# Kernel tuning notes

Measured on AMD Instinct MI355X. Metric: run time of the kernel, lower is better.

## Reference

```python
import jax, jax.numpy as jnp
import numpy as np

DIM = 128
DIM_OUT = 128
TK = 3   # time kernel (causal)
SK = 3   # spatial kernel
EPS = 1e-8


def setup_inputs() -> dict:
    key = jax.random.key(0)
    k1, k2, k3 = jax.random.split(key, 3)
    fmap = jax.random.normal(k1, (4, DIM, 16, 64, 64), dtype=jnp.float32)
    cond = jax.random.normal(k2, (4, DIM), dtype=jnp.float32)
    fan_in = DIM * TK * SK * SK
    gain = 0.75  # kaiming gain for selu
    weights = jax.random.normal(k3, (DIM_OUT, DIM, TK, SK, SK), dtype=jnp.float32) * (gain / np.sqrt(fan_in))
    return {"fmap": fmap, "cond": cond, "weights": weights}


def reference(fmap, cond, weights):
    # per-sample weight modulation: w[b,o,i,kt,kh,kw] = W[o,i,...] * (cond[b,i] + 1)
    w = weights[None] * (cond[:, None, :, None, None, None] + 1.0)
    # demodulation: normalize per (b, o) over (i, kt, kh, kw)
    ssq = jnp.sum(w * w, axis=(2, 3, 4, 5), keepdims=True)
    w = w * jax.lax.rsqrt(jnp.maximum(ssq, EPS))
    # causal time padding (TK-1, 0), symmetric spatial padding SK//2
    sp = SK // 2
    fmap_p = jnp.pad(fmap, ((0, 0), (0, 0), (TK - 1, 0), (sp, sp), (sp, sp)))
    # per-sample conv3d (equivalent to groups=b grouped conv)
    dn = ('NCDHW', 'OIDHW', 'NCDHW')
    def conv_one(x, wi):
        # x: [c, t, h, w], wi: [o, i, kt, kh, kw]
        return jax.lax.conv_general_dilated(
            x[None], wi, window_strides=(1, 1, 1), padding='VALID',
            dimension_numbers=dn)[0]
    return jax.vmap(conv_one)(fmap_p, w)  # [b, o, t, h, w]
```

## Files before the change

kernel.cpp:

```cpp
#include <hip/hip_runtime.h>

typedef float f32x4 __attribute__((ext_vector_type(4)));
typedef short s16x8 __attribute__((ext_vector_type(8)));

#define NB 4
#define CIN 128
#define COUT 128
#define NT 16
#define NH 64
#define NW 64
#define NTAP 27
#define KTOT (CIN * NTAP)

#define FT_H 66
#define FT_W 66
#define WMOD_BYTES (NB * NTAP * COUT * CIN * 2)
#define FT_U16 ((size_t)NB * NT * FT_H * FT_W * CIN)
#define FT_BYTES (FT_U16 * 2)
#define WS_NEED ((size_t)WMOD_BYTES + FT_BYTES)

#define SFT 4
#define SFH 6
#define SFW 72
#define SFPX (SFT * SFH * SFW)
#define SF_SLOTS (SFPX * 4)
#define SW_U16 (COUT * 32)

__device__ __forceinline__ unsigned short f32_to_bf16(float f) {
    unsigned int u = __builtin_bit_cast(unsigned int, f);
    u += 0x7FFFu + ((u >> 16) & 1u);
    return (unsigned short)(u >> 16);
}

__device__ __forceinline__ void gload16(const void* g, void* l) {
    __builtin_amdgcn_global_load_lds(
        (const __attribute__((address_space(1))) unsigned int*)g,
        (__attribute__((address_space(3))) unsigned int*)l, 16, 0, 0);
}

__global__ __launch_bounds__(256) void modw_kernel(
    const float* __restrict__ cond,
    const float* __restrict__ weights,
    unsigned short* __restrict__ wmod,
    int swz)
{
    int bo = blockIdx.x;
    int b = bo >> 7;
    int o = bo & 127;
    int tid = threadIdx.x;
    __shared__ float red[256];
    __shared__ float s_scale;
    const float* wrow = weights + o * KTOT;
    const float* cb = cond + b * CIN;

    float acc = 0.f;
    for (int idx = tid; idx < KTOT; idx += 256) {
        int i = idx / NTAP;
        float v = wrow[idx] * (cb[i] + 1.0f);
        acc += v * v;
    }
    red[tid] = acc;
    __syncthreads();
    #pragma unroll
    for (int s = 128; s > 0; s >>= 1) {
        if (tid < s) red[tid] += red[tid + s];
        __syncthreads();
    }
    if (tid == 0) s_scale = 1.0f / sqrtf(fmaxf(red[0], 1e-8f));
    __syncthreads();
    float scale = s_scale;
    int sw_o = swz ? ((o >> 1) & 3) : 0;

    for (int idx = tid; idx < KTOT; idx += 256) {
        int i = idx / NTAP;
        int tap = idx - i * NTAP;
        float v = wrow[idx] * (cb[i] + 1.0f) * scale;
        int pos = (i & 0x60) | ((((i >> 3) & 3) ^ sw_o) << 3) | (i & 7);
        wmod[(((b * NTAP + tap) * COUT + o) * CIN) + pos] = f32_to_bf16(v);
    }
}

__global__ void border_kernel(unsigned short* __restrict__ fmapT) {
    int idx = blockIdx.x * blockDim.x + threadIdx.x;
    int total = NB * NT * 260 * 16;
    if (idx >= total) return;
    int slot = idx & 15;
    int pid = idx >> 4;
    int r = pid % 260;
    int bt = pid / 260;
    int hh, ww;
    if (r < 66)       { hh = 0;  ww = r; }
    else if (r < 132) { hh = 65; ww = r - 66; }
    else if (r < 196) { ww = 0;  hh = r - 131; }
    else              { ww = 65; hh = r - 195; }
    size_t p = (((size_t)bt * FT_H + hh) * FT_W + ww) * CIN + slot * 8;
    uint4 z = {0, 0, 0, 0};
    *reinterpret_cast<uint4*>(&fmapT[p]) = z;
}

__global__ __launch_bounds__(256) void transpose_kernel(
    const float* __restrict__ fmap, unsigned short* __restrict__ fmapT)
{
    __shared__ __attribute__((aligned(16))) unsigned short sT[NW * 136];
    int bid = blockIdx.x;
    int h = bid & 63;
    int t = (bid >> 6) & 15;
    int b = bid >> 10;
    int tid = threadIdx.x;

    int c = tid >> 1, wh = (tid & 1) * 32;
    const float* src = fmap + (((size_t)(b * CIN + c) * NT + t) * NH + h) * NW + wh;
    #pragma unroll
    for (int j = 0; j < 8; ++j) {
        float4 v = *reinterpret_cast<const float4*>(src + j * 4);
        int w = wh + j * 4;
        sT[(w + 0) * 136 + c] = f32_to_bf16(v.x);
        sT[(w + 1) * 136 + c] = f32_to_bf16(v.y);
        sT[(w + 2) * 136 + c] = f32_to_bf16(v.z);
        sT[(w + 3) * 136 + c] = f32_to_bf16(v.w);
    }
    __syncthreads();

    int w = tid >> 2, qq = tid & 3;
    int sw = ((w + 1) >> 1) & 3;
    size_t pixbase = (((size_t)(b * NT + t) * FT_H + (h + 1)) * FT_W + (w + 1)) * CIN;
    #pragma unroll
    for (int s = 0; s < 4; ++s) {
        int g = qq * 4 + s;
        uint4 v = *reinterpret_cast<const uint4*>(&sT[w * 136 + g * 8]);
        int slot = (g & 12) | ((g & 3) ^ sw);
        *reinterpret_cast<uint4*>(&fmapT[pixbase + slot * 8]) = v;
    }
}

__global__ __launch_bounds__(512, 2) void conv2_kernel(
    const unsigned short* __restrict__ fmapT,
    const unsigned short* __restrict__ wmod,
    float* __restrict__ out)
{
    __shared__ __attribute__((aligned(16))) unsigned short sF[SFPX * 32];
    __shared__ __attribute__((aligned(16))) unsigned short sW[2][SW_U16];

    int obid = blockIdx.x;
    int bid = (obid & 7) * 64 + (obid >> 3);
    int h0 = (bid & 15) * 4;
    int t0 = ((bid >> 4) & 7) * 2;
    int b  = bid >> 7;

    int tid = threadIdx.x;
    int wv = tid >> 6;
    int l  = tid & 63;
    int lo = l & 15, hi = l >> 4;
    int obase = (wv & 1) * 64;
    int tsub  = (wv >> 1) & 1;
    int hp    = (wv >> 2) * 2;

    int swzA = (lo >> 1) & 3;

    f32x4 acc[4][2][4];
    f32x4 zz = {0.f, 0.f, 0.f, 0.f};
    #pragma unroll
    for (int a = 0; a < 4; ++a)
        #pragma unroll
        for (int h2 = 0; h2 < 2; ++h2)
            #pragma unroll
            for (int p = 0; p < 4; ++p)
                acc[a][h2][p] = zz;

    int nz = (t0 == 0) ? (2 * SFH * SFW * 4) : 0;

    auto stage_f = [&](int ic) {
        #pragma unroll 1
        for (int j = 0; j < 14; ++j) {
            int s = j * 512 + tid;
            if (s < SF_SLOTS) {
                int px = s >> 2, q = s & 3;
                int row = px / SFW;
                int wl = px - row * SFW;
                int tl = row / SFH;
                int hl = row - tl * SFH;
                int ts = t0 + tl - 2; if (ts < 0) ts = 0;
                int wlc = wl > 65 ? 65 : wl;
                const unsigned short* src = fmapT +
                    ((((size_t)(b * NT + ts) * FT_H + (h0 + hl)) * FT_W + wlc) << 7)
                    + (ic << 5) + (q << 3);
                gload16(src, &sF[(size_t)s * 8]);
            }
        }
    };
    auto stage_w = [&](int buf, int tap, int ic) {
        const unsigned short* src = wmod +
            (((size_t)(b * NTAP + tap) * COUT + (tid >> 2)) << 7)
            + (ic << 5) + ((tid & 3) << 3);
        gload16(src, &sW[buf][tid * 8]);
    };
    auto zero_t = [&]() {
        uint4 z = {0, 0, 0, 0};
        for (int s = tid; s < nz; s += 512)
            *reinterpret_cast<uint4*>(&sF[s * 8]) = z;
    };

    stage_f(0);
    stage_w(0, 0, 0);
    asm volatile("s_waitcnt vmcnt(0)" ::: "memory");
    if (nz) zero_t();
    __syncthreads();

    int tap = 0, kt = 0, kh = 0, kw = 0, ic = 0;
    for (int ks = 0; ks < 108; ++ks) {
        int cur = ks & 1;
        bool last_tap = (tap == NTAP - 1);
        if (!last_tap)
            stage_w(cur ^ 1, tap + 1, ic);

        int swzB = ((lo + kw) >> 1) & 3;
        const unsigned short* wb = &sW[cur][((obase + lo) << 5) + ((hi ^ swzA) << 3)];
        s16x8 af[4];
        #pragma unroll
        for (int a = 0; a < 4; ++a)
            af[a] = *reinterpret_cast<const s16x8*>(&wb[a << 9]);

        #pragma unroll
        for (int h2 = 0; h2 < 2; ++h2) {
            int row = (tsub + kt) * SFH + hp + h2 + kh;
            int pix = row * SFW + kw + lo;
            const unsigned short* fb = &sF[(pix << 5) + ((hi ^ swzB) << 3)];
            s16x8 bf[4];
            #pragma unroll
            for (int p = 0; p < 4; ++p)
                bf[p] = *reinterpret_cast<const s16x8*>(&fb[p << 9]);
            #pragma unroll
            for (int a = 0; a < 4; ++a)
                #pragma unroll
                for (int p = 0; p < 4; ++p)
                    acc[a][h2][p] = __builtin_amdgcn_mfma_f32_16x16x32_bf16(
                        af[a], bf[p], acc[a][h2][p], 0, 0, 0);
        }

        if (!last_tap) {
            ++tap; ++kw;
            if (kw == 3) { kw = 0; ++kh; if (kh == 3) { kh = 0; ++kt; } }
            asm volatile("s_waitcnt vmcnt(0)" ::: "memory");
            __syncthreads();
        } else {
            __syncthreads();
            if (ks < 107) {
                ++ic;
                stage_f(ic);
                stage_w(cur ^ 1, 0, ic);
                asm volatile("s_waitcnt vmcnt(0)" ::: "memory");
                if (nz) zero_t();
                __syncthreads();
            }
            tap = 0; kw = 0; kh = 0; kt = 0;
        }
    }

    int t = t0 + tsub;
    #pragma unroll
    for (int a = 0; a < 4; ++a) {
        #pragma unroll
        for (int h2 = 0; h2 < 2; ++h2) {
            int h = h0 + hp + h2;
            #pragma unroll
            for (int reg = 0; reg < 4; ++reg) {
                int o = obase + a * 16 + hi * 4 + reg;
                float* orow = out + ((((size_t)b * COUT + o) * NT + t) * NH + h) * NW;
                #pragma unroll
                for (int p = 0; p < 4; ++p)
                    orow[p * 16 + lo] = acc[a][h2][p][reg];
            }
        }
    }
}

#define HB 4
#define SF_T 3
#define SF_Hf (HB + 2)
#define SF_Wf (NW + 2)
#define IPAD 40
#define SPATf (SF_T * SF_Hf * SF_Wf)

__global__ __launch_bounds__(512) void conv_kernel(
    const float* __restrict__ fmap,
    const unsigned short* __restrict__ wmod,
    float* __restrict__ out)
{
    __shared__ unsigned short sFf[SPATf * IPAD];
    __shared__ unsigned short sWf[2][COUT * IPAD];

    int bid = blockIdx.x;
    int h0 = (bid & 15) * HB;
    int t0 = (bid >> 4) & 15;
    int b  = bid >> 8;

    int tid = threadIdx.x;
    int wv = tid >> 6;
    int l  = tid & 63;
    int lo = l & 15;
    int hi = l >> 4;
    int obase = (wv & 1) * 64;
    int r = wv >> 1;

    int s_ii = tid >> 4;
    int s_ws = tid & 15;

    f32x4 acc[4][4];
    #pragma unroll
    for (int a = 0; a < 4; ++a)
        #pragma unroll
        for (int p = 0; p < 4; ++p)
            acc[a][p] = f32x4{0.f, 0.f, 0.f, 0.f};

    int tap = 0, icc = 0;
    for (int ks = 0; ks < 108; ++ks) {
        if (tap == 0) {
            if (ks) __syncthreads();
            const float* fbase = fmap + (size_t)((b * CIN + icc * 32 + s_ii) * NT) * (NH * NW);
            for (int e = s_ws; e < SPATf; e += 16) {
                int wl = e % SF_Wf;
                int rr = e / SF_Wf;
                int hl = rr % SF_Hf;
                int tl = rr / SF_Hf;
                int ts = t0 + tl - 2;
                int hs = h0 + hl - 1;
                int wsrc = wl - 1;
                float v = 0.f;
                if (ts >= 0 && (unsigned)hs < NH && (unsigned)wsrc < NW)
                    v = fbase[(ts * NH + hs) * NW + wsrc];
                sFf[e * IPAD + s_ii] = f32_to_bf16(v);
            }
            if (ks == 0) {
                int o = tid >> 2, q = tid & 3;
                const unsigned short* src =
                    wmod + (((b * NTAP + 0) * COUT + o) * CIN) + q * 8;
                *reinterpret_cast<uint4*>(&sWf[0][o * IPAD + q * 8]) =
                    *reinterpret_cast<const uint4*>(src);
            }
        }
        __syncthreads();

        if (ks + 1 < 108) {
            int ksn = ks + 1;
            int icn = ksn / 27;
            int tapn = ksn - icn * 27;
            int o = tid >> 2, q = tid & 3;
            const unsigned short* src =
                wmod + (((b * NTAP + tapn) * COUT + o) * CIN) + icn * 32 + q * 8;
            *reinterpret_cast<uint4*>(&sWf[ksn & 1][o * IPAD + q * 8]) =
                *reinterpret_cast<const uint4*>(src);
        }

        int kt = tap / 9;
        int rem = tap - kt * 9;
        int kh = rem / 3;
        int kw = rem - kh * 3;

        s16x8 af[4], bfr[4];
        #pragma unroll
        for (int a = 0; a < 4; ++a) {
            int o = obase + a * 16 + lo;
            af[a] = *reinterpret_cast<const s16x8*>(&sWf[ks & 1][o * IPAD + hi * 8]);
        }
        #pragma unroll
        for (int p = 0; p < 4; ++p) {
            int sp = (kt * SF_Hf + (r + kh)) * SF_Wf + (p * 16 + lo + kw);
            bfr[p] = *reinterpret_cast<const s16x8*>(&sFf[sp * IPAD + hi * 8]);
        }
        #pragma unroll
        for (int a = 0; a < 4; ++a)
            #pragma unroll
            for (int p = 0; p < 4; ++p)
                acc[a][p] = __builtin_amdgcn_mfma_f32_16x16x32_bf16(
                    af[a], bfr[p], acc[a][p], 0, 0, 0);

        if (++tap == 27) { tap = 0; ++icc; }
    }

    int h = h0 + r;
    #pragma unroll
    for (int a = 0; a < 4; ++a) {
        #pragma unroll
        for (int reg = 0; reg < 4; ++reg) {
            int o = obase + a * 16 + hi * 4 + reg;
            float* orow = out + ((((size_t)b * COUT + o) * NT + t0) * NH + h) * NW;
            #pragma unroll
            for (int p = 0; p < 4; ++p)
                orow[p * 16 + lo] = acc[a][p][reg];
        }
    }
}

extern "C" void kernel_launch(void* const* d_in, const int* in_sizes, int n_in,
                              void* d_out, int out_size, void* d_ws, size_t ws_size,
                              hipStream_t stream) {
    (void)in_sizes; (void)n_in; (void)out_size;
    const float* fmap    = (const float*)d_in[0];
    const float* cond    = (const float*)d_in[1];
    const float* weights = (const float*)d_in[2];
    float* outp = (float*)d_out;
    unsigned short* wmod = (unsigned short*)d_ws;

    if (ws_size >= WS_NEED) {
        unsigned short* fmapT = (unsigned short*)((char*)d_ws + WMOD_BYTES);
        modw_kernel<<<dim3(NB * COUT), dim3(256), 0, stream>>>(cond, weights, wmod, 1);
        border_kernel<<<dim3((NB * NT * 260 * 16 + 255) / 256), dim3(256), 0, stream>>>(fmapT);
        transpose_kernel<<<dim3(NB * NT * NH), dim3(256), 0, stream>>>(fmap, fmapT);
        conv2_kernel<<<dim3(NB * (NT / 2) * (NH / 4)), dim3(512), 0, stream>>>(fmapT, wmod, outp);
    } else {
        modw_kernel<<<dim3(NB * COUT), dim3(256), 0, stream>>>(cond, weights, wmod, 0);
        conv_kernel<<<dim3(NB * NT * (NH / HB)), dim3(512), 0, stream>>>(fmap, wmod, outp);
    }
}
```

Measured before the change: 298.6 us.

## Triple-buffer weight tiles with vmcnt(1) prefetch and trim feature tile width

Weight staging moves from double to triple buffering, with loads issued two steps ahead. Waits use vmcnt(1) plus raw s_barrier instead of a full drain and __syncthreads, so one weight load can remain in flight while the MFMAs run. The feature tile width shrinks from 72 to 66 columns, which cuts staged bytes and LDS use and removes the column clamp. s_setprio is raised around the MFMA block. The exchange is more LDS spent on the third weight buffer and more delicate wait-count ordering, since the feature stage and the weight prefetch now interleave.

```diff
diff --git a/kernel.cpp b/kernel.cpp
--- a/kernel.cpp
+++ b/kernel.cpp
@@ -21,10 +21,15 @@
 
 #define SFT 4
 #define SFH 6
-#define SFW 72
+#define SFW 66
 #define SFPX (SFT * SFH * SFW)
 #define SF_SLOTS (SFPX * 4)
 #define SW_U16 (COUT * 32)
+
+#define VMCNT1() asm volatile("s_waitcnt vmcnt(1)" ::: "memory")
+#define VMCNT0() asm volatile("s_waitcnt vmcnt(0)" ::: "memory")
+#define LGKM0()  asm volatile("s_waitcnt lgkmcnt(0)" ::: "memory")
+#define BARRIER() asm volatile("s_barrier" ::: "memory")
 
 __device__ __forceinline__ unsigned short f32_to_bf16(float f) {
     unsigned int u = __builtin_bit_cast(unsigned int, f);
@@ -139,7 +144,7 @@
     float* __restrict__ out)
 {
     __shared__ __attribute__((aligned(16))) unsigned short sF[SFPX * 32];
-    __shared__ __attribute__((aligned(16))) unsigned short sW[2][SW_U16];
+    __shared__ __attribute__((aligned(16))) unsigned short sW[3][SW_U16];
 
     int obid = blockIdx.x;
     int bid = (obid & 7) * 64 + (obid >> 3);
@@ -171,7 +176,7 @@
 
     auto stage_f = [&](int ic) {
         #pragma unroll 1
-        for (int j = 0; j < 14; ++j) {
+        for (int j = 0; j < 13; ++j) {
             int s = j * 512 + tid;
             if (s < SF_SLOTS) {
                 int px = s >> 2, q = s & 3;
@@ -179,39 +184,54 @@
                 int wl = px - row * SFW;
                 int tl = row / SFH;
                 int hl = row - tl * SFH;
-                int ts = t0 + tl - 2; if (ts < 0) ts = 0;
-                int wlc = wl > 65 ? 65 : wl;
+                int ts = t0 + tl - 2;
+                if (ts < 0) ts = 0;
                 const unsigned short* src = fmapT +
-                    ((((size_t)(b * NT + ts) * FT_H + (h0 + hl)) * FT_W + wlc) << 7)
+                    ((((size_t)(b * NT + ts) * FT_H + (h0 + hl)) * FT_W + wl) << 7)
                     + (ic << 5) + (q << 3);
                 gload16(src, &sF[(size_t)s * 8]);
             }
         }
     };
-    auto stage_w = [&](int buf, int tap, int ic) {
+    auto stage_w = [&](int j) {
+        if (j > 107) j = 107;
+        int icw = j / 27;
+        int tapw = j - icw * 27;
         const unsigned short* src = wmod +
-            (((size_t)(b * NTAP + tap) * COUT + (tid >> 2)) << 7)
-            + (ic << 5) + ((tid & 3) << 3);
-        gload16(src, &sW[buf][tid * 8]);
+            (((size_t)(b * NTAP + tapw) * COUT + (tid >> 2)) << 7)
+            + (icw << 5) + ((tid & 3) << 3);
+        gload16(src, &sW[j % 3][tid * 8]);
     };
     auto zero_t = [&]() {
         uint4 z = {0, 0, 0, 0};
         for (int s = tid; s < nz; s += 512)
-            *reinterpret_cast<uint4*>(&sF[s * 8]) = z;
+            *reinterpret_cast<uint4*>(&sF[(size_t)s * 8]) = z;
     };
 
     stage_f(0);
-    stage_w(0, 0, 0);
-    asm volatile("s_waitcnt vmcnt(0)" ::: "memory");
+    stage_w(0);
+    stage_w(1);
+    VMCNT0();
     if (nz) zero_t();
-    __syncthreads();
-
-    int tap = 0, kt = 0, kh = 0, kw = 0, ic = 0;
+    LGKM0();
+    BARRIER();
+
+    int tap = 0, kt = 0, kh = 0, kw = 0, ic = 0, cur = 0;
     for (int ks = 0; ks < 108; ++ks) {
-        int cur = ks & 1;
-        bool last_tap = (tap == NTAP - 1);
-        if (!last_tap)
-            stage_w(cur ^ 1, tap + 1, ic);
+        if (tap == 0 && ks) {
+            VMCNT1(); LGKM0();
+            BARRIER();
+            stage_f(ic);
+            stage_w(ks + 2);
+            VMCNT1();
+            if (nz) zero_t();
+            LGKM0();
+            BARRIER();
+        } else {
+            VMCNT1(); LGKM0();
+            BARRIER();
+            stage_w(ks + 2);
+        }
 
         int swzB = ((lo + kw) >> 1) & 3;
         const unsigned short* wb = &sW[cur][((obase + lo) << 5) + ((hi ^ swzA) << 3)];
@@ -220,6 +240,7 @@
         for (int a = 0; a < 4; ++a)
             af[a] = *reinterpret_cast<const s16x8*>(&wb[a << 9]);
 
+        __builtin_amdgcn_s_setprio(1);
         #pragma unroll
         for (int h2 = 0; h2 < 2; ++h2) {
             int row = (tsub + kt) * SFH + hp + h2 + kh;
@@ -236,24 +257,12 @@
                     acc[a][h2][p] = __builtin_amdgcn_mfma_f32_16x16x32_bf16(
                         af[a], bf[p], acc[a][h2][p], 0, 0, 0);
         }
-
-        if (!last_tap) {
-            ++tap; ++kw;
-            if (kw == 3) { kw = 0; ++kh; if (kh == 3) { kh = 0; ++kt; } }
-            asm volatile("s_waitcnt vmcnt(0)" ::: "memory");
-            __syncthreads();
-        } else {
-            __syncthreads();
-            if (ks < 107) {
-                ++ic;
-                stage_f(ic);
-                stage_w(cur ^ 1, 0, ic);
-                asm volatile("s_waitcnt vmcnt(0)" ::: "memory");
-                if (nz) zero_t();
-                __syncthreads();
-            }
-            tap = 0; kw = 0; kh = 0; kt = 0;
-        }
+        __builtin_amdgcn_s_setprio(0);
+
+        ++tap; ++kw;
+        if (kw == 3) { kw = 0; ++kh; if (kh == 3) { kh = 0; ++kt; } }
+        if (tap == NTAP) { tap = 0; kw = 0; kh = 0; kt = 0; ++ic; }
+        cur = (cur == 2) ? 0 : cur + 1;
     }
 
     int t = t0 + tsub;
```

Result: no change. 303.2 us (+1.5%).
